# Kernel tuning notes

Measured on AMD Instinct MI355X. Metric: run time of the kernel, lower is better.

The kernel has to match this reference:

```python
import jax, jax.numpy as jnp
import numpy as np

GROUPS = 32
EPS = 1e-5


def group_norm(x, gamma, beta):
    # x: [B, C, H, W]; normalize over (C//G, H, W) within each of G groups
    B, C, H, W = x.shape
    xg = x.reshape(B, GROUPS, C // GROUPS, H, W)
    mean = xg.mean(axis=(2, 3, 4), keepdims=True)
    var = xg.var(axis=(2, 3, 4), keepdims=True)
    xg = (xg - mean) * jax.lax.rsqrt(var + EPS)
    x = xg.reshape(B, C, H, W)
    return x * gamma[None, :, None, None] + beta[None, :, None, None]


def conv1x1(x, W, b):
    # 1x1 conv == pointwise linear over channels. x: [B,C,H,W], W: [Cout,Cin]
    return jnp.einsum('oc,bchw->bohw', W, x) + b[None, :, None, None]


def setup_inputs() -> dict:
    key = jax.random.key(0)
    ks = jax.random.split(key, 6)
    B, C, H, W = 16, 512, 32, 32
    scale = 1.0 / np.sqrt(C)  # ~kaiming-ish init for 1x1 convs
    return {
        'x': jax.random.normal(ks[0], (B, C, H, W), jnp.float32),
        'gn_gamma': jnp.ones((C,), jnp.float32),
        'gn_beta': jnp.zeros((C,), jnp.float32),
        'Wq': jax.random.normal(ks[1], (C, C), jnp.float32) * scale,
        'bq': jnp.zeros((C,), jnp.float32),
        'Wk': jax.random.normal(ks[2], (C, C), jnp.float32) * scale,
        'bk': jnp.zeros((C,), jnp.float32),
        'Wv': jax.random.normal(ks[3], (C, C), jnp.float32) * scale,
        'bv': jnp.zeros((C,), jnp.float32),
        'Wp': jax.random.normal(ks[4], (C, C), jnp.float32) * scale,
        'bp': jnp.zeros((C,), jnp.float32),
    }


def reference(x, gn_gamma, gn_beta, Wq, bq, Wk, bk, Wv, bv, Wp, bp):
    B, C, H, W = x.shape
    h = group_norm(x, gn_gamma, gn_beta)
    q = conv1x1(h, Wq, bq).reshape(B, C, H * W)  # [B,C,T]
    k = conv1x1(h, Wk, bk).reshape(B, C, H * W)
    v = conv1x1(h, Wv, bv).reshape(B, C, H * W)
    # scores [B, T(query), S(key)] = q^T k, scaled by C^{-1/2}
    w = jnp.einsum('bct,bcs->bts', q, k) * (C ** -0.5)
    w = jax.nn.softmax(w, axis=-1)
    h = jnp.einsum('bts,bcs->bct', w, v).reshape(B, C, H, W)
    h = conv1x1(h, Wp, bp)
    return x + h
```

## Files before the change

### kernel.cpp

```cpp
#include <hip/hip_runtime.h>

typedef unsigned short u16;
typedef __bf16 bf16x8 __attribute__((ext_vector_type(8)));
typedef float f32x4 __attribute__((ext_vector_type(4)));

__device__ __forceinline__ u16 f2bf(float f) {
    unsigned u = __builtin_bit_cast(unsigned, f);
    u += 0x7fffu + ((u >> 16) & 1u);
    return (u16)(u >> 16);
}
__device__ __forceinline__ float bf2f(u16 h) {
    return __builtin_bit_cast(float, (unsigned)h << 16);
}

#define GLDS16(g, l) __builtin_amdgcn_global_load_lds( \
    (const __attribute__((address_space(1))) void*)(g), \
    (__attribute__((address_space(3))) void*)(l), 16, 0, 0)

#define QK_SCALE 0.044194173824159216f

__global__ __launch_bounds__(256) void convert_kernel(
    const float* __restrict__ Wq, const float* __restrict__ Wk,
    const float* __restrict__ Wv, const float* __restrict__ Wp,
    const float* __restrict__ bq, const float* __restrict__ bk,
    const float* __restrict__ bv,
    u16* __restrict__ Wqkv, u16* __restrict__ Wpb, float* __restrict__ bqkv)
{
    int idx = blockIdx.x * 256 + threadIdx.x;
    if (idx < 786432) {
        int which = idx >> 18;
        int off   = idx & 262143;
        if (which == 0)
            Wqkv[idx] = f2bf(Wq[off] * QK_SCALE);
        else
            Wqkv[idx] = f2bf(((which == 1) ? Wk : Wv)[off]);
    } else {
        int off = idx - 786432;
        Wpb[off] = f2bf(Wp[off]);
    }
    if (idx < 1536) {
        float bvv = (idx < 512) ? bq[idx] * QK_SCALE
                  : (idx < 1024) ? bk[idx & 511] : bv[idx & 511];
        bqkv[idx] = bvv;
    }
}

__global__ __launch_bounds__(256) void gn_stats(
    const float* __restrict__ x, float2* __restrict__ stats)
{
    const int g = blockIdx.x, b = blockIdx.y, tid = threadIdx.x;
    const float* xg = x + ((size_t)b * 512 + (size_t)g * 16) * 1024;

    float s = 0.f, s2 = 0.f;
    const float4* x4 = (const float4*)xg;
    #pragma unroll 4
    for (int i = tid; i < 4096; i += 256) {
        float4 v = x4[i];
        s  += v.x + v.y + v.z + v.w;
        s2 += v.x * v.x + v.y * v.y + v.z * v.z + v.w * v.w;
    }
    #pragma unroll
    for (int off = 32; off; off >>= 1) {
        s  += __shfl_down(s, off);
        s2 += __shfl_down(s2, off);
    }
    __shared__ float rs[4], rs2[4];
    const int w = tid >> 6;
    if ((tid & 63) == 0) { rs[w] = s; rs2[w] = s2; }
    __syncthreads();
    if (tid == 0) {
        float S  = rs[0] + rs[1] + rs[2] + rs[3];
        float S2 = rs2[0] + rs2[1] + rs2[2] + rs2[3];
        float mean = S * (1.f / 16384.f);
        float var  = S2 * (1.f / 16384.f) - mean * mean;
        stats[b * 32 + g] = make_float2(mean, rsqrtf(var + 1e-5f));
    }
}

__global__ __launch_bounds__(256) void gn_apply(
    const float* __restrict__ x, const float* __restrict__ gamma,
    const float* __restrict__ beta, const float2* __restrict__ stats,
    u16* __restrict__ ht)
{
    const int tc = blockIdx.x, b = blockIdx.y, tid = threadIdx.x;
    const int t0 = tc * 32;

    __shared__ float2 st[32];
    __shared__ float ga[512], be[512];
    __shared__ __align__(16) u16 tile[512 * 32];

    if (tid < 32) st[tid] = stats[b * 32 + tid];
    for (int c = tid; c < 512; c += 256) { ga[c] = gamma[c]; be[c] = beta[c]; }
    __syncthreads();

    #pragma unroll
    for (int pass = 0; pass < 16; pass++) {
        const int c = pass * 32 + (tid >> 3);
        const int f = tid & 7;
        float4 v = *(const float4*)(x + ((size_t)(b * 512 + c)) * 1024 + t0 + f * 4);
        float2 s = st[c >> 4];
        float sc = s.y * ga[c];
        float sh = be[c] - s.x * sc;
        ushort4 hv = {f2bf(v.x * sc + sh), f2bf(v.y * sc + sh),
                      f2bf(v.z * sc + sh), f2bf(v.w * sc + sh)};
        const int slot = f ^ (c & 7) ^ ((c >> 3) & 7);
        *(ushort4*)(tile + c * 32 + slot * 4) = hv;
    }
    __syncthreads();

    #pragma unroll
    for (int p = 0; p < 8; p++) {
        const int t = p * 4 + (tid >> 6);
        const int l = tid & 63;
        u16 tmp[8];
        #pragma unroll
        for (int e = 0; e < 8; e++) {
            const int c = l * 8 + e;
            const int slot = (t >> 2) ^ (c & 7) ^ ((c >> 3) & 7);
            tmp[e] = tile[c * 32 + slot * 4 + (t & 3)];
        }
        *(uint4*)(ht + ((size_t)b * 1024 + t0 + t) * 512 + l * 8) = *(uint4*)tmp;
    }
}

__global__ __launch_bounds__(512, 2) void flash64(
    const u16* __restrict__ q,
    const u16* __restrict__ k,
    const u16* __restrict__ v,
    u16* __restrict__ o)
{
    __shared__ __align__(16) u16 smem[66688];

    const int tid  = threadIdx.x;
    const int lane = tid & 63;
    const int wave = tid >> 6;
    const int l15  = lane & 15;
    const int lh   = lane >> 4;
    const int rx   = lane & 7;

    const int flat  = blockIdx.x;
    const int b     = ((flat & 7) << 1) | (flat >> 7);
    const int qtile = (flat >> 3) & 15;
    const int t0    = qtile * 64;

    const u16* Qg = q + ((size_t)b * 1024 + t0) * 512;
    const u16* Kg = k + (size_t)b * 524288;
    const u16* Vg = v + (size_t)b * 524288;
    u16*       Og = o + ((size_t)b * 1024 + t0) * 512;

    #pragma unroll
    for (int u = 0; u < 8; u++) {
        const int r0 = wave + 8 * u;
        GLDS16(Qg + r0 * 512 + (lane ^ (r0 & 7)) * 8,
               smem + r0 * 512 + lane * 8);
    }
    asm volatile("s_waitcnt vmcnt(0)" ::: "memory");
    __syncthreads();

    f32x4 oacc[4][4] = {};
    float rs_[16] = {};

    for (int st = 0; st < 4; st++) {
        u16* Pc = smem + 32768 + (st & 1) * 16384;
        const u16* Kst = Kg + (size_t)(st * 256) * 512;
        f32x4 sacc[4][2] = {};

        #pragma unroll
        for (int i = 0; i < 16; i++) {
            bf16x8 af[4], bfr[2];
            #pragma unroll
            for (int mi = 0; mi < 4; mi++)
                af[mi] = *(const bf16x8*)(smem + (mi * 16 + l15) * 512 +
                                          (((i * 4 + lh) ^ rx) << 3));
            #pragma unroll
            for (int nj = 0; nj < 2; nj++)
                bfr[nj] = *(const bf16x8*)(Kst +
                          (size_t)(wave * 32 + nj * 16 + l15) * 512 + i * 32 + lh * 8);
            __builtin_amdgcn_s_setprio(1);
            #pragma unroll
            for (int mi = 0; mi < 4; mi++)
                #pragma unroll
                for (int nj = 0; nj < 2; nj++)
                    sacc[mi][nj] = __builtin_amdgcn_mfma_f32_16x16x32_bf16(
                        af[mi], bfr[nj], sacc[mi][nj], 0, 0, 0);
            __builtin_amdgcn_s_setprio(0);
        }

        #pragma unroll
        for (int mi = 0; mi < 4; mi++) {
            #pragma unroll
            for (int nj = 0; nj < 2; nj++) {
                #pragma unroll
                for (int r = 0; r < 4; r++) {
                    float e = __expf(sacc[mi][nj][r]);
                    u16 h = f2bf(e);
                    rs_[mi * 4 + r] += bf2f(h);
                    const int tr = mi * 16 + lh * 4 + r;
                    const int s  = wave * 32 + nj * 16 + l15;
                    Pc[tr * 256 + (((s >> 3) ^ (tr & 7)) << 3) + (s & 7)] = h;
                }
            }
        }
        asm volatile("s_waitcnt lgkmcnt(0)" ::: "memory");
        __builtin_amdgcn_s_barrier();

        const u16* Vst = Vg + st * 256;
        #pragma unroll
        for (int j = 0; j < 8; j++) {
            bf16x8 pa[4], vb[4];
            #pragma unroll
            for (int mi = 0; mi < 4; mi++)
                pa[mi] = *(const bf16x8*)(Pc + (mi * 16 + l15) * 256 +
                                          (((j * 4 + lh) ^ rx) << 3));
            #pragma unroll
            for (int nj = 0; nj < 4; nj++)
                vb[nj] = *(const bf16x8*)(Vst +
                         (size_t)(wave * 64 + nj * 16 + l15) * 1024 + j * 32 + lh * 8);
            __builtin_amdgcn_s_setprio(1);
            #pragma unroll
            for (int mi = 0; mi < 4; mi++)
                #pragma unroll
                for (int nj = 0; nj < 4; nj++)
                    oacc[mi][nj] = __builtin_amdgcn_mfma_f32_16x16x32_bf16(
                        pa[mi], vb[nj], oacc[mi][nj], 0, 0, 0);
            __builtin_amdgcn_s_setprio(0);
        }
    }

    float* rl = (float*)(smem + 65536);
    #pragma unroll
    for (int i = 0; i < 16; i++) {
        rs_[i] += __shfl_xor(rs_[i], 1);
        rs_[i] += __shfl_xor(rs_[i], 2);
        rs_[i] += __shfl_xor(rs_[i], 4);
        rs_[i] += __shfl_xor(rs_[i], 8);
    }
    if (l15 == 0) {
        #pragma unroll
        for (int mi = 0; mi < 4; mi++)
            #pragma unroll
            for (int r = 0; r < 4; r++)
                rl[wave * 64 + mi * 16 + lh * 4 + r] = rs_[mi * 4 + r];
    }
    __syncthreads();
    if (tid < 64) {
        float tot = 0.f;
        #pragma unroll
        for (int w = 0; w < 8; w++) tot += rl[w * 64 + tid];
        rl[512 + tid] = 1.0f / tot;
    }
    __syncthreads();
    float ri_[16];
    #pragma unroll
    for (int mi = 0; mi < 4; mi++)
        #pragma unroll
        for (int r = 0; r < 4; r++)
            ri_[mi * 4 + r] = rl[512 + mi * 16 + lh * 4 + r];
    #pragma unroll
    for (int mi = 0; mi < 4; mi++)
        #pragma unroll
        for (int nj = 0; nj < 4; nj++)
            #pragma unroll
            for (int r = 0; r < 4; r++)
                Og[(size_t)(mi * 16 + lh * 4 + r) * 512 + wave * 64 + nj * 16 + l15]
                    = f2bf(oacc[mi][nj][r] * ri_[mi * 4 + r]);
}

template <int MODE>
__global__ __launch_bounds__(512, 2) void gemm_nt(
    const u16* __restrict__ A, const u16* __restrict__ B,
    size_t strideA, size_t strideB, int lda, int ldb, int K,
    u16* __restrict__ o0, u16* __restrict__ o1, u16* __restrict__ o2,
    float* __restrict__ fo, const float* __restrict__ bias,
    const float* __restrict__ xres)
{
    __shared__ __align__(16) u16 smem[73728];
    u16* As = smem;
    u16* Bs = smem + 49152;

    const int tid  = threadIdx.x;
    const int lane = tid & 63;
    const int wave = tid >> 6;
    const int wm   = (wave & 3) * 64;
    const int wn   = (wave >> 2) * 64;

    const int gx = gridDim.x, gy = gridDim.y;
    int f = blockIdx.x + gx * (blockIdx.y + gy * blockIdx.z);
    const int nwg = gx * gy * (int)gridDim.z;
    f = (f & 7) * (nwg >> 3) + (f >> 3);
    const int bx  = f % gx;
    const int byz = f / gx;
    const int by  = byz % gy;
    const int b   = byz / gy;

    const u16* Ab = A + (size_t)b * strideA + (size_t)by * 256 * lda;
    const u16* Bb = B + (size_t)b * strideB + (size_t)bx * 128 * ldb;

    const int srow = tid >> 3;
    const int sc   = tid & 7;
    const int scg  = sc ^ (srow & 7);

    const u16* aSrc[4]; int aDst[4];
    #pragma unroll
    for (int u = 0; u < 4; u++) {
        aSrc[u] = Ab + (size_t)(u * 64 + srow) * lda + scg * 8;
        aDst[u] = (u * 64 + srow) * 64 + sc * 8;
    }
    const u16* bSrc[2]; int bDst[2];
    #pragma unroll
    for (int u = 0; u < 2; u++) {
        bSrc[u] = Bb + (size_t)(u * 64 + srow) * ldb + scg * 8;
        bDst[u] = (u * 64 + srow) * 64 + sc * 8;
    }

    const int l15 = lane & 15, lh = lane >> 4, rx = lane & 7;
    int aOff[4][2], bOff[4][2];
    #pragma unroll
    for (int i = 0; i < 4; i++)
        #pragma unroll
        for (int ks = 0; ks < 2; ks++) {
            const int slot = ((ks << 2) + lh) ^ rx;
            aOff[i][ks] = (wm + i * 16 + l15) * 64 + slot * 8;
            bOff[i][ks] = (wn + i * 16 + l15) * 64 + slot * 8;
        }

    f32x4 acc[4][4] = {};
    const int NT = K >> 6;

    #pragma unroll
    for (int u = 0; u < 4; u++) GLDS16(aSrc[u], As + aDst[u]);
    #pragma unroll
    for (int u = 0; u < 2; u++) GLDS16(bSrc[u], Bs + bDst[u]);
    #pragma unroll
    for (int u = 0; u < 4; u++) GLDS16(aSrc[u] + 64, As + 16384 + aDst[u]);
    #pragma unroll
    for (int u = 0; u < 2; u++) GLDS16(bSrc[u] + 64, Bs + 8192 + bDst[u]);

    int cbuf = 0, sbuf = 2;
    for (int t = 0; t < NT; ++t) {
        if (t == NT - 1) asm volatile("s_waitcnt vmcnt(0)" ::: "memory");
        else             asm volatile("s_waitcnt vmcnt(6)" ::: "memory");
        __builtin_amdgcn_s_barrier();

        const u16* Ac = As + cbuf * 16384;
        const u16* Bc = Bs + cbuf * 8192;
        u16* Asb = As + sbuf * 16384;
        u16* Bsb = Bs + sbuf * 8192;
        const int ko = (t + 2) * 64;
        const bool pf = (t + 2 < NT);

        if (pf) {
            GLDS16(aSrc[0] + ko, Asb + aDst[0]);
            GLDS16(aSrc[1] + ko, Asb + aDst[1]);
            GLDS16(bSrc[0] + ko, Bsb + bDst[0]);
        }
        {
            bf16x8 af[4], bfr[4];
            #pragma unroll
            for (int i = 0; i < 4; i++) {
                af[i]  = *(const bf16x8*)(Ac + aOff[i][0]);
                bfr[i] = *(const bf16x8*)(Bc + bOff[i][0]);
            }
            __builtin_amdgcn_s_setprio(1);
            #pragma unroll
            for (int mi = 0; mi < 4; mi++)
                #pragma unroll
                for (int nj = 0; nj < 4; nj++)
                    acc[mi][nj] = __builtin_amdgcn_mfma_f32_16x16x32_bf16(
                        af[mi], bfr[nj], acc[mi][nj], 0, 0, 0);
            __builtin_amdgcn_s_setprio(0);
        }
        if (pf) {
            GLDS16(aSrc[2] + ko, Asb + aDst[2]);
            GLDS16(aSrc[3] + ko, Asb + aDst[3]);
            GLDS16(bSrc[1] + ko, Bsb + bDst[1]);
        }
        {
            bf16x8 af[4], bfr[4];
            #pragma unroll
            for (int i = 0; i < 4; i++) {
                af[i]  = *(const bf16x8*)(Ac + aOff[i][1]);
                bfr[i] = *(const bf16x8*)(Bc + bOff[i][1]);
            }
            __builtin_amdgcn_s_setprio(1);
            #pragma unroll
            for (int mi = 0; mi < 4; mi++)
                #pragma unroll
                for (int nj = 0; nj < 4; nj++)
                    acc[mi][nj] = __builtin_amdgcn_mfma_f32_16x16x32_bf16(
                        af[mi], bfr[nj], acc[mi][nj], 0, 0, 0);
            __builtin_amdgcn_s_setprio(0);
        }

        cbuf = (cbuf == 2) ? 0 : cbuf + 1;
        sbuf = (sbuf == 2) ? 0 : sbuf + 1;
    }

    const int N0 = bx * 128;
    const int M0 = by * 256;

    if (MODE == 0 && N0 < 1024) {
        u16* dst = (N0 < 512) ? o0 : o1;
        const int nn0 = N0 & 511;
        #pragma unroll
        for (int nj = 0; nj < 4; nj++) {
            const int n = wn + nj * 16 + l15;
            const float bv = bias[N0 + n];
            #pragma unroll
            for (int mi = 0; mi < 4; mi++) {
                const int mq = M0 + wm + mi * 16 + lh * 4;
                const size_t base = ((size_t)b * 1024 + mq) * 512 + nn0 + n;
                dst[base]        = f2bf(acc[mi][nj][0] + bv);
                dst[base + 512]  = f2bf(acc[mi][nj][1] + bv);
                dst[base + 1024] = f2bf(acc[mi][nj][2] + bv);
                dst[base + 1536] = f2bf(acc[mi][nj][3] + bv);
            }
        }
    } else if (MODE == 0) {
        __syncthreads();
        #pragma unroll
        for (int mi = 0; mi < 4; mi++) {
            const int mq = wm + mi * 16 + lh * 4;
            #pragma unroll
            for (int nj = 0; nj < 4; nj++) {
                const int n = wn + nj * 16 + l15;
                const float bv = bias[N0 + n];
                ushort4 hv = {f2bf(acc[mi][nj][0] + bv), f2bf(acc[mi][nj][1] + bv),
                              f2bf(acc[mi][nj][2] + bv), f2bf(acc[mi][nj][3] + bv)};
                *(ushort4*)((char*)smem + n * 512 +
                            (((mq >> 3) ^ (n & 31)) << 4) + ((mq >> 2) & 1) * 8) = hv;
            }
        }
        __syncthreads();
        #pragma unroll
        for (int p = 0; p < 8; p++) {
            const int n  = p * 16 + (tid >> 5);
            const int gi = tid & 31;
            uint4 v4 = *(const uint4*)((char*)smem + n * 512 +
                                       ((gi ^ (n & 31)) << 4));
            u16* dst = o2 + ((size_t)b * 512 + (N0 - 1024) + n) * 1024 + M0;
            *(uint4*)(dst + gi * 8) = v4;
        }
    } else {
        __syncthreads();
        float* smf = (float*)smem;
        #pragma unroll
        for (int mi = 0; mi < 4; mi++) {
            const int mq = wm + mi * 16 + lh * 4;
            #pragma unroll
            for (int nj = 0; nj < 4; nj++) {
                const int n = wn + nj * 16 + l15;
                float4 v4 = {acc[mi][nj][0], acc[mi][nj][1],
                             acc[mi][nj][2], acc[mi][nj][3]};
                *(float4*)((char*)smf + n * 1024 +
                           (((mq >> 2) ^ (n & 63)) << 4)) = v4;
            }
        }
        __syncthreads();
        #pragma unroll
        for (int p = 0; p < 16; p++) {
            const int n  = p * 8 + (tid >> 6);
            const int gi = tid & 63;
            float4 v4 = *(const float4*)((char*)smf + n * 1024 +
                                         ((gi ^ (n & 63)) << 4));
            const size_t off = ((size_t)b * 512 + N0 + n) * 1024 + M0 + gi * 4;
            const float bv = bias[N0 + n];
            const float4 xv = *(const float4*)(xres + off);
            float4 ov = {v4.x + bv + xv.x, v4.y + bv + xv.y,
                         v4.z + bv + xv.z, v4.w + bv + xv.w};
            *(float4*)(fo + off) = ov;
        }
    }
}

extern "C" void kernel_launch(void* const* d_in, const int* in_sizes, int n_in,
                              void* d_out, int out_size, void* d_ws, size_t ws_size,
                              hipStream_t stream)
{
    const float* x     = (const float*)d_in[0];
    const float* gamma = (const float*)d_in[1];
    const float* beta  = (const float*)d_in[2];
    const float* Wq    = (const float*)d_in[3];
    const float* bq    = (const float*)d_in[4];
    const float* Wk    = (const float*)d_in[5];
    const float* bk    = (const float*)d_in[6];
    const float* Wv    = (const float*)d_in[7];
    const float* bv    = (const float*)d_in[8];
    const float* Wp    = (const float*)d_in[9];
    const float* bp    = (const float*)d_in[10];

    char* ws = (char*)d_ws;
    u16*   Wqkv   = (u16*)(ws + 0);
    u16*   Wpb    = (u16*)(ws + 1572864);
    float* bqkv   = (float*)(ws + 2097152);
    u16*   ht     = (u16*)(ws + 2105344);
    u16*   kt     = (u16*)(ws + 18882560);
    u16*   vv     = (u16*)(ws + 35659776);
    u16*   qt  = (u16*)d_out;
    float2* stats = (float2*)((char*)d_out + 16777216);
    u16*   h2  = ht;
    float* out = (float*)d_out;

    convert_kernel<<<4096, 256, 0, stream>>>(Wq, Wk, Wv, Wp, bq, bk, bv,
                                             Wqkv, Wpb, bqkv);
    gn_stats<<<dim3(32, 16), 256, 0, stream>>>(x, stats);
    gn_apply<<<dim3(32, 16), 256, 0, stream>>>(x, gamma, beta, stats, ht);

    gemm_nt<0><<<dim3(12, 4, 16), 512, 0, stream>>>(
        ht, Wqkv, 524288, 0, 512, 512, 512,
        qt, kt, vv, nullptr, bqkv, nullptr);

    flash64<<<256, 512, 0, stream>>>(qt, kt, vv, h2);

    gemm_nt<3><<<dim3(4, 4, 16), 512, 0, stream>>>(
        h2, Wpb, 524288, 0, 512, 512, 512,
        nullptr, nullptr, nullptr, out, bp, x);
}
```

Measured before the change: 236.2 us.

## Restructure flash attention kernel to 16 waves with transposed MFMA and staged output

The attention kernel moves from 512 to 1024 threads per block, so each of 16 waves owns a 16-key slice for the scores and a 32-channel slice for P·V. The MFMA operands are swapped: K and V rows become the A operand and Q and P tiles the B operand. That lets P be written to shared memory as packed 4-element vectors and the output be staged through swizzled LDS for coalesced 16-byte global stores. K and V global loads are software-prefetched one step ahead. The aim is more latency hiding and fewer scattered scalar stores, at the cost of per-thread register pressure under the 1024-thread launch bound, and the row-sum reduction is reworked to match.

```diff
diff --git a/kernel.cpp b/kernel.cpp
--- a/kernel.cpp
+++ b/kernel.cpp
@@ -123,20 +123,20 @@
     }
 }
 
-__global__ __launch_bounds__(512, 2) void flash64(
+__global__ __launch_bounds__(1024) void flash64(
     const u16* __restrict__ q,
     const u16* __restrict__ k,
     const u16* __restrict__ v,
     u16* __restrict__ o)
 {
-    __shared__ __align__(16) u16 smem[66688];
+    __shared__ __align__(16) u16 smem[67712];
 
     const int tid  = threadIdx.x;
     const int lane = tid & 63;
     const int wave = tid >> 6;
     const int l15  = lane & 15;
     const int lh   = lane >> 4;
-    const int rx   = lane & 7;
+    const int r7   = l15 & 7;
 
     const int flat  = blockIdx.x;
     const int b     = ((flat & 7) << 1) | (flat >> 7);
@@ -149,121 +149,140 @@
     u16*       Og = o + ((size_t)b * 1024 + t0) * 512;
 
     #pragma unroll
-    for (int u = 0; u < 8; u++) {
-        const int r0 = wave + 8 * u;
+    for (int u = 0; u < 4; u++) {
+        const int r0 = wave + 16 * u;
         GLDS16(Qg + r0 * 512 + (lane ^ (r0 & 7)) * 8,
                smem + r0 * 512 + lane * 8);
     }
     asm volatile("s_waitcnt vmcnt(0)" ::: "memory");
     __syncthreads();
 
-    f32x4 oacc[4][4] = {};
-    float rs_[16] = {};
+    f32x4 oacc[2][4] = {};
+    float rs_[4] = {};
 
     for (int st = 0; st < 4; st++) {
         u16* Pc = smem + 32768 + (st & 1) * 16384;
-        const u16* Kst = Kg + (size_t)(st * 256) * 512;
-        f32x4 sacc[4][2] = {};
-
+
+        f32x4 sacc[4] = {};
+        const u16* Krow = Kg + (size_t)(st * 256 + wave * 16 + l15) * 512 + lh * 8;
+        bf16x8 kf = *(const bf16x8*)(Krow);
         #pragma unroll
         for (int i = 0; i < 16; i++) {
-            bf16x8 af[4], bfr[2];
-            #pragma unroll
-            for (int mi = 0; mi < 4; mi++)
-                af[mi] = *(const bf16x8*)(smem + (mi * 16 + l15) * 512 +
-                                          (((i * 4 + lh) ^ rx) << 3));
-            #pragma unroll
-            for (int nj = 0; nj < 2; nj++)
-                bfr[nj] = *(const bf16x8*)(Kst +
-                          (size_t)(wave * 32 + nj * 16 + l15) * 512 + i * 32 + lh * 8);
+            bf16x8 kn;
+            if (i < 15) kn = *(const bf16x8*)(Krow + (i + 1) * 32);
+            bf16x8 qf[4];
+            #pragma unroll
+            for (int nj = 0; nj < 4; nj++)
+                qf[nj] = *(const bf16x8*)(smem + (nj * 16 + l15) * 512 +
+                                          (((i * 4 + lh) ^ r7) << 3));
             __builtin_amdgcn_s_setprio(1);
             #pragma unroll
-            for (int mi = 0; mi < 4; mi++)
-                #pragma unroll
-                for (int nj = 0; nj < 2; nj++)
-                    sacc[mi][nj] = __builtin_amdgcn_mfma_f32_16x16x32_bf16(
-                        af[mi], bfr[nj], sacc[mi][nj], 0, 0, 0);
+            for (int nj = 0; nj < 4; nj++)
+                sacc[nj] = __builtin_amdgcn_mfma_f32_16x16x32_bf16(
+                    kf, qf[nj], sacc[nj], 0, 0, 0);
             __builtin_amdgcn_s_setprio(0);
-        }
-
-        #pragma unroll
-        for (int mi = 0; mi < 4; mi++) {
-            #pragma unroll
-            for (int nj = 0; nj < 2; nj++) {
-                #pragma unroll
-                for (int r = 0; r < 4; r++) {
-                    float e = __expf(sacc[mi][nj][r]);
-                    u16 h = f2bf(e);
-                    rs_[mi * 4 + r] += bf2f(h);
-                    const int tr = mi * 16 + lh * 4 + r;
-                    const int s  = wave * 32 + nj * 16 + l15;
-                    Pc[tr * 256 + (((s >> 3) ^ (tr & 7)) << 3) + (s & 7)] = h;
-                }
-            }
+            if (i < 15) kf = kn;
+        }
+
+        const int sb   = wave * 16 + lh * 4;
+        const int gsl  = (sb >> 3);
+        const int ghl  = (sb & 7) * 2;
+        #pragma unroll
+        for (int nj = 0; nj < 4; nj++) {
+            const int t = nj * 16 + l15;
+            u16 hv[4];
+            #pragma unroll
+            for (int r = 0; r < 4; r++) {
+                float e = __expf(sacc[nj][r]);
+                u16 h = f2bf(e);
+                rs_[nj] += bf2f(h);
+                hv[r] = h;
+            }
+            *(ushort4*)((char*)Pc + t * 512 + ((gsl ^ (t & 7)) << 4) + ghl)
+                = *(ushort4*)hv;
         }
         asm volatile("s_waitcnt lgkmcnt(0)" ::: "memory");
         __builtin_amdgcn_s_barrier();
 
-        const u16* Vst = Vg + st * 256;
+        const u16* Vrow0 = Vg + (size_t)(wave * 32 + l15) * 1024 + st * 256 + lh * 8;
+        const u16* Vrow1 = Vrow0 + 16 * 1024;
+        bf16x8 va0 = *(const bf16x8*)(Vrow0);
+        bf16x8 va1 = *(const bf16x8*)(Vrow1);
         #pragma unroll
         for (int j = 0; j < 8; j++) {
-            bf16x8 pa[4], vb[4];
-            #pragma unroll
-            for (int mi = 0; mi < 4; mi++)
-                pa[mi] = *(const bf16x8*)(Pc + (mi * 16 + l15) * 256 +
-                                          (((j * 4 + lh) ^ rx) << 3));
-            #pragma unroll
-            for (int nj = 0; nj < 4; nj++)
-                vb[nj] = *(const bf16x8*)(Vst +
-                         (size_t)(wave * 64 + nj * 16 + l15) * 1024 + j * 32 + lh * 8);
+            bf16x8 na0, na1;
+            if (j < 7) {
+                na0 = *(const bf16x8*)(Vrow0 + (j + 1) * 32);
+                na1 = *(const bf16x8*)(Vrow1 + (j + 1) * 32);
+            }
+            bf16x8 pb[4];
+            #pragma unroll
+            for (int nj = 0; nj < 4; nj++) {
+                const int t = nj * 16 + l15;
+                pb[nj] = *(const bf16x8*)((char*)Pc + t * 512 +
+                                          (((j * 4 + lh) ^ (t & 7)) << 4));
+            }
             __builtin_amdgcn_s_setprio(1);
             #pragma unroll
-            for (int mi = 0; mi < 4; mi++)
-                #pragma unroll
-                for (int nj = 0; nj < 4; nj++)
-                    oacc[mi][nj] = __builtin_amdgcn_mfma_f32_16x16x32_bf16(
-                        pa[mi], vb[nj], oacc[mi][nj], 0, 0, 0);
+            for (int nj = 0; nj < 4; nj++) {
+                oacc[0][nj] = __builtin_amdgcn_mfma_f32_16x16x32_bf16(
+                    va0, pb[nj], oacc[0][nj], 0, 0, 0);
+                oacc[1][nj] = __builtin_amdgcn_mfma_f32_16x16x32_bf16(
+                    va1, pb[nj], oacc[1][nj], 0, 0, 0);
+            }
             __builtin_amdgcn_s_setprio(0);
-        }
-    }
-
-    float* rl = (float*)(smem + 65536);
-    #pragma unroll
-    for (int i = 0; i < 16; i++) {
-        rs_[i] += __shfl_xor(rs_[i], 1);
-        rs_[i] += __shfl_xor(rs_[i], 2);
-        rs_[i] += __shfl_xor(rs_[i], 4);
-        rs_[i] += __shfl_xor(rs_[i], 8);
-    }
-    if (l15 == 0) {
-        #pragma unroll
-        for (int mi = 0; mi < 4; mi++)
-            #pragma unroll
-            for (int r = 0; r < 4; r++)
-                rl[wave * 64 + mi * 16 + lh * 4 + r] = rs_[mi * 4 + r];
+            if (j < 7) { va0 = na0; va1 = na1; }
+        }
+    }
+
+    float* rl   = (float*)(smem + 65536);
+    float* rinv = rl + 1024;
+    #pragma unroll
+    for (int nj = 0; nj < 4; nj++) {
+        rs_[nj] += __shfl_xor(rs_[nj], 16);
+        rs_[nj] += __shfl_xor(rs_[nj], 32);
+    }
+    if (lane < 16) {
+        #pragma unroll
+        for (int nj = 0; nj < 4; nj++)
+            rl[wave * 64 + nj * 16 + lane] = rs_[nj];
     }
     __syncthreads();
     if (tid < 64) {
         float tot = 0.f;
         #pragma unroll
-        for (int w = 0; w < 8; w++) tot += rl[w * 64 + tid];
-        rl[512 + tid] = 1.0f / tot;
-    }
-    __syncthreads();
-    float ri_[16];
-    #pragma unroll
-    for (int mi = 0; mi < 4; mi++)
-        #pragma unroll
-        for (int r = 0; r < 4; r++)
-            ri_[mi * 4 + r] = rl[512 + mi * 16 + lh * 4 + r];
-    #pragma unroll
-    for (int mi = 0; mi < 4; mi++)
-        #pragma unroll
-        for (int nj = 0; nj < 4; nj++)
-            #pragma unroll
-            for (int r = 0; r < 4; r++)
-                Og[(size_t)(mi * 16 + lh * 4 + r) * 512 + wave * 64 + nj * 16 + l15]
-                    = f2bf(oacc[mi][nj][r] * ri_[mi * 4 + r]);
+        for (int w = 0; w < 16; w++) tot += rl[w * 64 + tid];
+        rinv[tid] = 1.0f / tot;
+    }
+    __syncthreads();
+
+    float ri_[4];
+    #pragma unroll
+    for (int nj = 0; nj < 4; nj++) ri_[nj] = rinv[nj * 16 + l15];
+
+    #pragma unroll
+    for (int mi = 0; mi < 2; mi++) {
+        const int cb  = wave * 32 + mi * 16 + lh * 4;
+        const int gsl = cb >> 3;
+        const int ghl = (cb & 7) * 2;
+        #pragma unroll
+        for (int nj = 0; nj < 4; nj++) {
+            const int t = nj * 16 + l15;
+            ushort4 hv = {f2bf(oacc[mi][nj][0] * ri_[nj]),
+                          f2bf(oacc[mi][nj][1] * ri_[nj]),
+                          f2bf(oacc[mi][nj][2] * ri_[nj]),
+                          f2bf(oacc[mi][nj][3] * ri_[nj])};
+            *(ushort4*)((char*)smem + t * 1024 + ((gsl ^ (t & 7)) << 4) + ghl) = hv;
+        }
+    }
+    __syncthreads();
+    #pragma unroll
+    for (int p = 0; p < 4; p++) {
+        const int t  = p * 16 + (tid >> 6);
+        const int gi = tid & 63;
+        uint4 v4 = *(const uint4*)((char*)smem + t * 1024 + ((gi ^ (t & 7)) << 4));
+        *(uint4*)(Og + t * 512 + gi * 8) = v4;
+    }
 }
 
 template <int MODE>
@@ -510,7 +529,7 @@
         ht, Wqkv, 524288, 0, 512, 512, 512,
         qt, kt, vv, nullptr, bqkv, nullptr);
 
-    flash64<<<256, 512, 0, stream>>>(qt, kt, vv, h2);
+    flash64<<<256, 1024, 0, stream>>>(qt, kt, vv, h2);
 
     gemm_nt<3><<<dim3(4, 4, 16), 512, 0, stream>>>(
         h2, Wpb, 524288, 0, 512, 512, 512,
```

New measurement: 238.7 us. About the same (+1.0%).
